# Performance work log

Measured on AMD Instinct MI355X. Metric: run time of the kernel, lower is better.

## Reference

```python
import jax, jax.numpy as jnp
import numpy as np
from jax import lax

B, S, H = 32, 512, 128
NEG_INF = -1e30  # matches util.masked_softmax's large negative fill


def setup_inputs() -> dict:
    key = jax.random.key(0)
    ks = jax.random.split(key, 10)
    sc = 0.05
    vp = jax.random.normal(ks[0], (B, S, 2 * H), dtype=jnp.float32)
    # valid lengths in [S//2, S]; packed loop runs max(lengths) steps
    p_s_lengths = jax.random.randint(ks[1], (B,), S // 2, S + 1, dtype=jnp.int32)
    W_vP  = jax.random.normal(ks[2], (H, 2 * H), dtype=jnp.float32) * sc      # linear_vP.weight
    W_vPt = jax.random.normal(ks[3], (H, 2 * H), dtype=jnp.float32) * sc      # linear_vPt.weight
    w_vT  = jax.random.normal(ks[4], (H,), dtype=jnp.float32) * sc            # linear_vT.weight (1,H) -> vector
    W_g   = jax.random.normal(ks[5], (4 * H, 4 * H), dtype=jnp.float32) * sc  # g.weight
    W_ih  = jax.random.normal(ks[6], (3 * H, 4 * H), dtype=jnp.float32) * sc  # GRUCell.weight_ih
    W_hh  = jax.random.normal(ks[7], (3 * H, H), dtype=jnp.float32) * sc      # GRUCell.weight_hh
    b_ih  = jax.random.normal(ks[8], (3 * H,), dtype=jnp.float32) * sc
    b_hh  = jax.random.normal(ks[9], (3 * H,), dtype=jnp.float32) * sc
    return dict(vp=vp, p_s_lengths=p_s_lengths, W_vP=W_vP, W_vPt=W_vPt,
                w_vT=w_vT, W_g=W_g, W_ih=W_ih, W_hh=W_hh, b_ih=b_ih, b_hh=b_hh)


def _self_attn_rnn(vp, p_s_lengths, W_vP, W_vPt, w_vT, W_g, W_ih, W_hh, b_ih, b_hh):
    Bb, Ss, H2 = vp.shape
    Hh = H2 // 2
    s_idx = jnp.arange(Ss)

    # reverse_enc: reverse each sequence only over its valid prefix
    rev_idx = jnp.where(s_idx[None, :] < p_s_lengths[:, None],
                        p_s_lengths[:, None] - 1 - s_idx[None, :], s_idx[None, :])
    rev_vp = jnp.take_along_axis(vp, rev_idx[:, :, None], axis=1)

    bidir_vp = jnp.concatenate([vp, rev_vp], axis=0)       # (2B,S,2H) inputs per step
    vp2 = jnp.concatenate([vp, vp], axis=0)                 # (2B,S,2H) attention memory (forward order!)
    len2 = jnp.concatenate([p_s_lengths, p_s_lengths], 0)   # (2B,)

    keyp = jnp.einsum('bsd,hd->bsh', vp2, W_vP)             # precompute linear_vP(vp)
    seq_mask = s_idx[None, :] < len2[:, None]               # (2B,S)

    def step(h, inputs):
        x_t, active = inputs                                # (2B,2H), (2B,)
        q = x_t @ W_vPt.T                                   # (2B,H)
        logits = jnp.tanh(keyp + q[:, None, :]) @ w_vT      # (2B,S)
        a = jax.nn.softmax(jnp.where(seq_mask, logits, NEG_INF), axis=1)
        ct = jnp.einsum('bs,bsd->bd', a, vp2)               # (2B,2H)
        vpc = jnp.concatenate([x_t, ct], axis=-1)           # (2B,4H)
        gt = jax.nn.sigmoid(vpc @ W_g.T)
        xin = gt * vpc
        gi = xin @ W_ih.T + b_ih
        gh = h @ W_hh.T + b_hh
        ir, iz, inn = jnp.split(gi, 3, axis=-1)
        hr, hz, hn = jnp.split(gh, 3, axis=-1)
        r = jax.nn.sigmoid(ir + hr)
        z = jax.nn.sigmoid(iz + hz)
        n = jnp.tanh(inn + r * hn)
        h_new = (1.0 - z) * n + z * h
        # packed semantics: inactive (padded) slots keep zeros and never update again
        h_new = jnp.where(active[:, None], h_new, 0.0)
        return h_new, h_new

    xs = (jnp.swapaxes(bidir_vp, 0, 1), seq_mask.T)          # (S,2B,2H), (S,2B)
    h0 = jnp.zeros((2 * Bb, Hh), dtype=vp.dtype)
    _, hs = lax.scan(jax.checkpoint(step), h0, xs)           # hs: (S,2B,H)
    hp = jnp.swapaxes(hs, 0, 1)                              # (2B,S,H)
    # original concatenates fwd half and rev half on feature dim (rev half stays in reversed time order)
    return jnp.concatenate([hp[:Bb], hp[Bb:]], axis=-1)      # (B,S,2H)


def reference(vp, p_s_lengths, W_vP, W_vPt, w_vT, W_g, W_ih, W_hh, b_ih, b_hh):
    # dropout is identity at inference (training=False)
    return _self_attn_rnn(vp, p_s_lengths, W_vP, W_vPt, w_vT, W_g, W_ih, W_hh, b_ih, b_hh)
```

## Files before the change

### kernel.cpp

```cpp
#include <hip/hip_runtime.h>
#include <hip/hip_fp16.h>

#define BB 32
#define SS 512
#define HH 128
#define D2 256
#define D3 384
#define D4 512

#define OFF_TK  0
#define OFF_TQ  (OFF_TK + BB*SS*HH)
#define OFF_CT  (OFF_TQ + BB*SS*HH)
#define OFF_GI  (OFF_CT + BB*SS*D2)
#define OFF_F16 (OFF_GI + BB*SS*D3)
#define F16_WG  0
#define F16_WIH (F16_WG + D4*D4)
#define F16_W2  (F16_WIH + D3*D4)

typedef _Float16 f16x8 __attribute__((ext_vector_type(8)));
typedef _Float16 f16x4 __attribute__((ext_vector_type(4)));
typedef float    f32x4 __attribute__((ext_vector_type(4)));
typedef _Float16 h2_t  __attribute__((ext_vector_type(2)));

__device__ __forceinline__ float fast_tanh(float x) {
  float ax = fabsf(x);
  float e  = __expf(-2.0f * ax);
  float t  = __fdividef(1.0f - e, 1.0f + e);
  return x < 0.0f ? -t : t;
}
__device__ __forceinline__ float sigm(float x) {
  return __fdividef(1.0f, 1.0f + __expf(-x));
}

__global__ __launch_bounds__(256) void k0_prep(
    const float* __restrict__ Wg, const float* __restrict__ Wih,
    const float* __restrict__ Wvp, const float* __restrict__ Wvpt,
    float* __restrict__ ws) {
  int i = blockIdx.x * 256 + threadIdx.x;
  _Float16* f16b = (_Float16*)(ws + OFF_F16);
  if (i < D4 * D4) {
    f16b[F16_WG + i] = (_Float16)Wg[i];
  } else if (i < D4 * D4 + D3 * D4) {
    int j = i - D4 * D4;
    f16b[F16_WIH + j] = (_Float16)Wih[j];
  } else {
    int j = i - D4 * D4 - D3 * D4;
    f16b[F16_W2 + j] = (_Float16)(j < HH * D2 ? Wvp[j] : Wvpt[j - HH * D2]);
  }
}

__global__ __launch_bounds__(256, 2) void k1_keyq(const float* __restrict__ vp,
                                                  float* __restrict__ ws) {
  __shared__ __align__(16) _Float16 vpH[64 * 256];
  int tid = threadIdx.x;
  int rows0 = blockIdx.x * 64;

  #pragma unroll
  for (int i = 0; i < 8; ++i) {
    int u = tid + i * 256;
    int r = u >> 5, c8 = u & 31;
    const float* src = vp + (size_t)(rows0 + r) * D2 + c8 * 8;
    float4 a = *(const float4*)src;
    float4 b = *(const float4*)(src + 4);
    f16x8 h;
    h[0]=(_Float16)a.x; h[1]=(_Float16)a.y; h[2]=(_Float16)a.z; h[3]=(_Float16)a.w;
    h[4]=(_Float16)b.x; h[5]=(_Float16)b.y; h[6]=(_Float16)b.z; h[7]=(_Float16)b.w;
    *(f16x8*)(&vpH[r * 256 + (c8 ^ (r & 7)) * 8]) = h;
  }
  __syncthreads();

  const _Float16* W2 = (const _Float16*)(ws + OFF_F16) + F16_W2;
  int w = tid >> 6, l = tid & 63;
  int lr = l & 15, lk = (l >> 4) * 8;

  f32x4 acc[4][4];
  #pragma unroll
  for (int m = 0; m < 4; ++m)
    #pragma unroll
    for (int n = 0; n < 4; ++n) acc[m][n] = (f32x4){0.f, 0.f, 0.f, 0.f};

  for (int kc = 0; kc < 8; ++kc) {
    int k = kc * 32 + lk;
    f16x8 bf[4];
    #pragma unroll
    for (int n = 0; n < 4; ++n) {
      int r = n * 16 + lr;
      bf[n] = *(const f16x8*)(&vpH[r * 256 + (((k >> 3) ^ (r & 7))) * 8]);
    }
    #pragma unroll
    for (int m = 0; m < 4; ++m) {
      int c = w * 64 + m * 16 + lr;
      f16x8 af = *(const f16x8*)(W2 + (size_t)c * 256 + k);
      #pragma unroll
      for (int n = 0; n < 4; ++n)
        acc[m][n] = __builtin_amdgcn_mfma_f32_16x16x32_f16(af, bf[n], acc[m][n], 0, 0, 0);
    }
  }

  int b = rows0 >> 9;
  int s0 = rows0 & 511;
  float* ekT = ws + OFF_TK + (size_t)b * HH * SS;
  float* eqp = ws + OFF_TQ + (size_t)b * SS * HH;
  #pragma unroll
  for (int m = 0; m < 4; ++m) {
    int c0 = w * 64 + m * 16 + (l >> 4) * 4;
    #pragma unroll
    for (int n = 0; n < 4; ++n) {
      int s = s0 + n * 16 + lr;
      float v[4];
      #pragma unroll
      for (int j = 0; j < 4; ++j) {
        float z = fminf(fmaxf(2.0f * acc[m][n][j], -60.0f), 60.0f);
        v[j] = __expf(z);
      }
      if (c0 < HH) {
        #pragma unroll
        for (int j = 0; j < 4; ++j)
          ekT[(size_t)(c0 + j) * SS + s] = v[j];
      } else {
        float4 o; o.x = v[0]; o.y = v[1]; o.z = v[2]; o.w = v[3];
        *(float4*)(eqp + (size_t)s * HH + (c0 - HH)) = o;
      }
    }
  }
}

__global__ __launch_bounds__(256) void k2_attn(const float* __restrict__ vp,
                                               const int* __restrict__ lens,
                                               const float* __restrict__ wvt,
                                               float* __restrict__ ws) {
  int bid = blockIdx.x;
  int b  = (bid & 7) * 4 + ((bid >> 3) & 3);
  int t0 = (bid >> 5) * 16;
  int len = lens[b];
  if (t0 >= len) return;
  int nt = min(16, len - t0);

  __shared__ float L[16][SS];
  __shared__ float Eqs[16][HH];
  __shared__ float inv_sum[16];

  int tid = threadIdx.x;
  const float* EkT = ws + OFF_TK + (size_t)b * HH * SS;
  const float* Eq  = ws + OFF_TQ + (size_t)b * SS * HH;

  for (int idx = tid; idx < 16 * HH; idx += 256) {
    int i = idx >> 7, h = idx & 127;
    Eqs[i][h] = Eq[(size_t)(t0 + i) * HH + h];
  }
  __syncthreads();

  for (int sc = 0; sc < 2; ++sc) {
    int s = tid + sc * 256;
    if (s < len) {
      float acc[16] = {};
      for (int h4 = 0; h4 < 32; ++h4) {
        float k0 = EkT[(size_t)(h4 * 4 + 0) * SS + s];
        float k1 = EkT[(size_t)(h4 * 4 + 1) * SS + s];
        float k2v = EkT[(size_t)(h4 * 4 + 2) * SS + s];
        float k3 = EkT[(size_t)(h4 * 4 + 3) * SS + s];
        const float4 w4 = *(const float4*)(wvt + h4 * 4);
        #pragma unroll
        for (int t = 0; t < 16; ++t) {
          const float4 q4 = *(const float4*)(&Eqs[t][h4 * 4]);
          float r0 = __builtin_amdgcn_rcpf(fmaf(k0, q4.x, 1.0f));
          float r1 = __builtin_amdgcn_rcpf(fmaf(k1, q4.y, 1.0f));
          float r2 = __builtin_amdgcn_rcpf(fmaf(k2v, q4.z, 1.0f));
          float r3 = __builtin_amdgcn_rcpf(fmaf(k3, q4.w, 1.0f));
          float a = acc[t];
          a = fmaf(w4.x, r0, a);
          a = fmaf(w4.y, r1, a);
          a = fmaf(w4.z, r2, a);
          a = fmaf(w4.w, r3, a);
          acc[t] = a;
        }
      }
      #pragma unroll
      for (int t = 0; t < 16; ++t) L[t][s] = -2.0f * acc[t];
    }
  }
  __syncthreads();

  {
    int w = tid >> 6, lane = tid & 63;
    for (int ii = 0; ii < 4; ++ii) {
      int i = w + ii * 4;
      if (i < nt) {
        float m = -1e30f;
        for (int s = lane; s < len; s += 64) m = fmaxf(m, L[i][s]);
        #pragma unroll
        for (int off = 32; off > 0; off >>= 1) m = fmaxf(m, __shfl_xor(m, off));
        float sm = 0.0f;
        for (int s = lane; s < len; s += 64) {
          float e = __expf(L[i][s] - m);
          L[i][s] = e;
          sm += e;
        }
        #pragma unroll
        for (int off = 32; off > 0; off >>= 1) sm += __shfl_xor(sm, off);
        if (lane == 0) inv_sum[i] = __fdividef(1.0f, sm);
      }
    }
  }
  __syncthreads();

  int d4 = (tid & 63) * 4;
  int tg = tid >> 6;
  float4 acc4[4] = {};
  const float* vpb = vp + (size_t)b * SS * D2;
  int s = 0;
  for (; s + 4 <= len; s += 4) {
    #pragma unroll
    for (int u = 0; u < 4; ++u) {
      float4 v4 = *(const float4*)(vpb + (size_t)(s + u) * D2 + d4);
      #pragma unroll
      for (int j = 0; j < 4; ++j) {
        float p = L[tg * 4 + j][s + u];
        acc4[j].x = fmaf(p, v4.x, acc4[j].x);
        acc4[j].y = fmaf(p, v4.y, acc4[j].y);
        acc4[j].z = fmaf(p, v4.z, acc4[j].z);
        acc4[j].w = fmaf(p, v4.w, acc4[j].w);
      }
    }
  }
  for (; s < len; ++s) {
    float4 v4 = *(const float4*)(vpb + (size_t)s * D2 + d4);
    #pragma unroll
    for (int j = 0; j < 4; ++j) {
      float p = L[tg * 4 + j][s];
      acc4[j].x = fmaf(p, v4.x, acc4[j].x);
      acc4[j].y = fmaf(p, v4.y, acc4[j].y);
      acc4[j].z = fmaf(p, v4.z, acc4[j].z);
      acc4[j].w = fmaf(p, v4.w, acc4[j].w);
    }
  }
  float* ctg = ws + OFF_CT + ((size_t)b * SS + t0) * D2;
  #pragma unroll
  for (int j = 0; j < 4; ++j) {
    int t = tg * 4 + j;
    if (t < nt) {
      float is = inv_sum[t];
      float4 o;
      o.x = acc4[j].x * is; o.y = acc4[j].y * is;
      o.z = acc4[j].z * is; o.w = acc4[j].w * is;
      *(float4*)(ctg + (size_t)t * D2 + d4) = o;
    }
  }
}

__global__ __launch_bounds__(256, 2) void k3_gates(const float* __restrict__ vp,
                                                   const int* __restrict__ lens,
                                                   const float* __restrict__ bih,
                                                   float* __restrict__ ws) {
  int b = blockIdx.y;
  int len = lens[b];
  int t0 = blockIdx.x * 32;
  if (t0 >= len) return;

  __shared__ __align__(16) _Float16 vpcH[32 * 512];
  int tid = threadIdx.x;
  const float* ct = ws + OFF_CT;

  #pragma unroll
  for (int i = 0; i < 8; ++i) {
    int u = tid + i * 256;
    int r = u >> 6, c8 = u & 63;
    int c = c8 * 8;
    const float* src = (c < D2) ? (vp + ((size_t)b * SS + t0 + r) * D2 + c)
                                : (ct + ((size_t)b * SS + t0 + r) * D2 + (c - D2));
    float4 a = *(const float4*)src;
    float4 bb = *(const float4*)(src + 4);
    f16x8 h;
    h[0]=(_Float16)a.x;  h[1]=(_Float16)a.y;  h[2]=(_Float16)a.z;  h[3]=(_Float16)a.w;
    h[4]=(_Float16)bb.x; h[5]=(_Float16)bb.y; h[6]=(_Float16)bb.z; h[7]=(_Float16)bb.w;
    *(f16x8*)(&vpcH[r * 512 + (c8 ^ (r & 7)) * 8]) = h;
  }
  __syncthreads();

  const _Float16* WgH  = (const _Float16*)(ws + OFF_F16) + F16_WG;
  const _Float16* WihH = (const _Float16*)(ws + OFF_F16) + F16_WIH;
  int w = tid >> 6, l = tid & 63;
  int lr = l & 15, lk = (l >> 4) * 8;

  f32x4 acc[8][2];
  #pragma unroll
  for (int m = 0; m < 8; ++m) { acc[m][0] = (f32x4){0.f,0.f,0.f,0.f}; acc[m][1] = (f32x4){0.f,0.f,0.f,0.f}; }

  for (int kc = 0; kc < 16; ++kc) {
    int k = kc * 32 + lk;
    f16x8 bf[2];
    #pragma unroll
    for (int n = 0; n < 2; ++n) {
      int r = n * 16 + lr;
      bf[n] = *(const f16x8*)(&vpcH[r * 512 + (((k >> 3) ^ (r & 7))) * 8]);
    }
    #pragma unroll
    for (int m = 0; m < 8; ++m) {
      int c = w * 128 + m * 16 + lr;
      f16x8 af = *(const f16x8*)(WgH + (size_t)c * 512 + k);
      acc[m][0] = __builtin_amdgcn_mfma_f32_16x16x32_f16(af, bf[0], acc[m][0], 0, 0, 0);
      acc[m][1] = __builtin_amdgcn_mfma_f32_16x16x32_f16(af, bf[1], acc[m][1], 0, 0, 0);
    }
  }

  f16x4 xq[8][2];
  #pragma unroll
  for (int m = 0; m < 8; ++m) {
    int c0 = w * 128 + m * 16 + (l >> 4) * 4;
    #pragma unroll
    for (int n = 0; n < 2; ++n) {
      int r = n * 16 + lr;
      int ea = r * 512 + (((c0 >> 3) ^ (r & 7))) * 8 + (c0 & 7);
      f16x4 vq = *(const f16x4*)(&vpcH[ea]);
      f16x4 xo;
      #pragma unroll
      for (int j = 0; j < 4; ++j)
        xo[j] = (_Float16)(sigm(acc[m][n][j]) * (float)vq[j]);
      xq[m][n] = xo;
    }
  }
  __syncthreads();
  #pragma unroll
  for (int m = 0; m < 8; ++m) {
    int c0 = w * 128 + m * 16 + (l >> 4) * 4;
    #pragma unroll
    for (int n = 0; n < 2; ++n) {
      int r = n * 16 + lr;
      int ea = r * 512 + (((c0 >> 3) ^ (r & 7))) * 8 + (c0 & 7);
      *(f16x4*)(&vpcH[ea]) = xq[m][n];
    }
  }
  __syncthreads();

  f32x4 gacc[6][2];
  #pragma unroll
  for (int m = 0; m < 6; ++m) { gacc[m][0] = (f32x4){0.f,0.f,0.f,0.f}; gacc[m][1] = (f32x4){0.f,0.f,0.f,0.f}; }

  for (int kc = 0; kc < 16; ++kc) {
    int k = kc * 32 + lk;
    f16x8 bf[2];
    #pragma unroll
    for (int n = 0; n < 2; ++n) {
      int r = n * 16 + lr;
      bf[n] = *(const f16x8*)(&vpcH[r * 512 + (((k >> 3) ^ (r & 7))) * 8]);
    }
    #pragma unroll
    for (int m = 0; m < 6; ++m) {
      int c = w * 96 + m * 16 + lr;
      f16x8 af = *(const f16x8*)(WihH + (size_t)c * 512 + k);
      gacc[m][0] = __builtin_amdgcn_mfma_f32_16x16x32_f16(af, bf[0], gacc[m][0], 0, 0, 0);
      gacc[m][1] = __builtin_amdgcn_mfma_f32_16x16x32_f16(af, bf[1], gacc[m][1], 0, 0, 0);
    }
  }

  float* gig = ws + OFF_GI;
  #pragma unroll
  for (int m = 0; m < 6; ++m) {
    int c0 = w * 96 + m * 16 + (l >> 4) * 4;
    float4 bq = *(const float4*)(bih + c0);
    #pragma unroll
    for (int n = 0; n < 2; ++n) {
      int r = n * 16 + lr;
      float4 o;
      o.x = gacc[m][n][0] + bq.x;
      o.y = gacc[m][n][1] + bq.y;
      o.z = gacc[m][n][2] + bq.z;
      o.w = gacc[m][n][3] + bq.w;
      *(float4*)(gig + ((size_t)b * SS + t0 + r) * D3 + c0) = o;
    }
  }
}

__global__ __launch_bounds__(256, 1) void k4_scan(const float* __restrict__ whh,
                                                  const float* __restrict__ bhh,
                                                  const int* __restrict__ lens,
                                                  const float* __restrict__ ws,
                                                  float* __restrict__ out) {
  int bid = blockIdx.x;
  int xcd = bid & 7, dir = (bid >> 3) & 1, q = bid >> 4;
  int b = xcd * 4 + q;
  int len = lens[b];
  int tid = threadIdx.x;
  int wv = tid >> 6, l = tid & 63;
  int j = wv * 32 + (l & 31);
  int p = l >> 5;
  const float* gi = ws + OFF_GI + (size_t)b * SS * D3;

  h2_t w0[32], w1[32], w2[32];
  {
    const float* r0 = whh + (size_t)j * HH + p * 64;
    const float* r1 = whh + (size_t)(j + 128) * HH + p * 64;
    const float* r2 = whh + (size_t)(j + 256) * HH + p * 64;
    #pragma unroll
    for (int k = 0; k < 32; ++k) {
      w0[k] = h2_t{(_Float16)r0[2 * k], (_Float16)r0[2 * k + 1]};
      w1[k] = h2_t{(_Float16)r1[2 * k], (_Float16)r1[2 * k + 1]};
      w2[k] = h2_t{(_Float16)r2[2 * k], (_Float16)r2[2 * k + 1]};
    }
  }
  float bh0 = bhh[j], bh1 = bhh[j + 128], bh2 = bhh[j + 256];

  __shared__ __align__(16) _Float16 hbuf[2][128];
  if (tid < 128) hbuf[0][tid] = (_Float16)0.0f;
  float h_own = 0.0f;

  float* outb = out + (size_t)b * SS * D2 + dir * HH;

#define K4_BAR() do {                                                          \
    asm volatile("s_waitcnt lgkmcnt(0)" ::: "memory");                         \
    __builtin_amdgcn_s_barrier();                                              \
    __builtin_amdgcn_sched_barrier(0);                                         \
  } while (0)

#define K4_PF(gx0, gx1, gx2, tnext) do {                                       \
    if (p == 0) {                                                              \
      int tp = (tnext) < len ? (tnext) : (len - 1);                            \
      int tgp = dir ? (len - 1 - tp) : tp;                                     \
      const float* gp = gi + (size_t)tgp * D3;                                 \
      gx0 = gp[j]; gx1 = gp[j + 128]; gx2 = gp[j + 256];                       \
    }                                                                          \
  } while (0)

#define K4_STEP(gx0, gx1, gx2, tstep, PB) do {                                 \
    const f16x8* hb8 = (const f16x8*)&hbuf[PB][p * 64];                        \
    float a00 = 0.f, a01 = 0.f, a02 = 0.f, a03 = 0.f;                          \
    float a10 = 0.f, a11 = 0.f, a12 = 0.f, a13 = 0.f;                          \
    float a20 = 0.f, a21 = 0.f, a22 = 0.f, a23 = 0.f;                          \
    _Pragma("unroll")                                                          \
    for (int k8 = 0; k8 < 8; ++k8) {                                           \
      f16x8 hv = hb8[k8];                                                      \
      h2_t q0 = __builtin_shufflevector(hv, hv, 0, 1);                         \
      h2_t q1 = __builtin_shufflevector(hv, hv, 2, 3);                         \
      h2_t q2 = __builtin_shufflevector(hv, hv, 4, 5);                         \
      h2_t q3 = __builtin_shufflevector(hv, hv, 6, 7);                         \
      a00 = __builtin_amdgcn_fdot2(q0, w0[4 * k8 + 0], a00, false);            \
      a01 = __builtin_amdgcn_fdot2(q1, w0[4 * k8 + 1], a01, false);            \
      a02 = __builtin_amdgcn_fdot2(q2, w0[4 * k8 + 2], a02, false);            \
      a03 = __builtin_amdgcn_fdot2(q3, w0[4 * k8 + 3], a03, false);            \
      a10 = __builtin_amdgcn_fdot2(q0, w1[4 * k8 + 0], a10, false);            \
      a11 = __builtin_amdgcn_fdot2(q1, w1[4 * k8 + 1], a11, false);            \
      a12 = __builtin_amdgcn_fdot2(q2, w1[4 * k8 + 2], a12, false);            \
      a13 = __builtin_amdgcn_fdot2(q3, w1[4 * k8 + 3], a13, false);            \
      a20 = __builtin_amdgcn_fdot2(q0, w2[4 * k8 + 0], a20, false);            \
      a21 = __builtin_amdgcn_fdot2(q1, w2[4 * k8 + 1], a21, false);            \
      a22 = __builtin_amdgcn_fdot2(q2, w2[4 * k8 + 2], a22, false);            \
      a23 = __builtin_amdgcn_fdot2(q3, w2[4 * k8 + 3], a23, false);            \
    }                                                                          \
    float s0 = ((a00 + a01) + (a02 + a03));                                    \
    float s1 = ((a10 + a11) + (a12 + a13));                                    \
    float s2 = ((a20 + a21) + (a22 + a23));                                    \
    s0 += __shfl_xor(s0, 32);                                                  \
    s1 += __shfl_xor(s1, 32);                                                  \
    s2 += __shfl_xor(s2, 32);                                                  \
    if (p == 0) {                                                              \
      float r = sigm((gx0) + s0 + bh0);                                        \
      float z = sigm((gx1) + s1 + bh1);                                        \
      float n = fast_tanh(fmaf(r, s2 + bh2, (gx2)));                           \
      float hn = (1.0f - z) * n + z * h_own;                                   \
      h_own = hn;                                                              \
      outb[(size_t)(tstep) * D2 + j] = hn;                                     \
      hbuf[(PB) ^ 1][j] = (_Float16)hn;                                        \
    }                                                                          \
    K4_PF(gx0, gx1, gx2, (tstep) + 4);                                         \
    K4_BAR();                                                                  \
  } while (0)

  float gA0 = 0.f, gA1 = 0.f, gA2 = 0.f;
  float gB0 = 0.f, gB1 = 0.f, gB2 = 0.f;
  float gC0 = 0.f, gC1 = 0.f, gC2 = 0.f;
  float gD0 = 0.f, gD1 = 0.f, gD2 = 0.f;
  K4_PF(gA0, gA1, gA2, 0);
  K4_PF(gB0, gB1, gB2, 1);
  K4_PF(gC0, gC1, gC2, 2);
  K4_PF(gD0, gD1, gD2, 3);
  K4_BAR();

  int t = 0;
  while (t + 3 < len) {
    K4_STEP(gA0, gA1, gA2, t,     0);
    K4_STEP(gB0, gB1, gB2, t + 1, 1);
    K4_STEP(gC0, gC1, gC2, t + 2, 0);
    K4_STEP(gD0, gD1, gD2, t + 3, 1);
    t += 4;
  }
  if (t < len)     K4_STEP(gA0, gA1, gA2, t,     0);
  if (t + 1 < len) K4_STEP(gB0, gB1, gB2, t + 1, 1);
  if (t + 2 < len) K4_STEP(gC0, gC1, gC2, t + 2, 0);

#undef K4_STEP
#undef K4_PF
#undef K4_BAR
}

extern "C" void kernel_launch(void* const* d_in, const int* in_sizes, int n_in,
                              void* d_out, int out_size, void* d_ws, size_t ws_size,
                              hipStream_t stream) {
  const float* vp   = (const float*)d_in[0];
  const int*   lens = (const int*)d_in[1];
  const float* Wvp  = (const float*)d_in[2];
  const float* Wvpt = (const float*)d_in[3];
  const float* wvt  = (const float*)d_in[4];
  const float* Wg   = (const float*)d_in[5];
  const float* Wih  = (const float*)d_in[6];
  const float* Whh  = (const float*)d_in[7];
  const float* bih  = (const float*)d_in[8];
  const float* bhh  = (const float*)d_in[9];
  float* out = (float*)d_out;
  float* ws  = (float*)d_ws;

  hipMemsetAsync(d_out, 0, (size_t)out_size * sizeof(float), stream);

  k0_prep<<<2048, 256, 0, stream>>>(Wg, Wih, Wvp, Wvpt, ws);
  k1_keyq<<<BB * SS / 64, 256, 0, stream>>>(vp, ws);
  k2_attn<<<1024, 256, 0, stream>>>(vp, lens, wvt, ws);
  k3_gates<<<dim3(SS / 32, BB), 256, 0, stream>>>(vp, lens, bih, ws);
  k4_scan<<<64, 256, 0, stream>>>(Whh, bhh, lens, ws, out);
}
```

Measured before the change: 530.8 us.

## Process forward and reverse GRU directions in one scan block per batch

The recurrent scan kernel now runs both directions for a batch in a single workgroup, so it launches 32 blocks instead of 64. Each step does two independent dot-product sets over separate shared h buffers and shares one barrier between them. This halves the number of barriers per step pair and gives each step two independent chains to interleave for latency hiding. The cost is a longer per-step critical path and half as many CUs in use, so the scan's wall time may grow if the chains do not overlap well.

```diff
diff --git a/kernel.cpp b/kernel.cpp
--- a/kernel.cpp
+++ b/kernel.cpp
@@ -377,8 +377,7 @@
                                                   const float* __restrict__ ws,
                                                   float* __restrict__ out) {
   int bid = blockIdx.x;
-  int xcd = bid & 7, dir = (bid >> 3) & 1, q = bid >> 4;
-  int b = xcd * 4 + q;
+  int b = (bid & 7) * 4 + (bid >> 3);
   int len = lens[b];
   int tid = threadIdx.x;
   int wv = tid >> 6, l = tid & 63;
@@ -400,11 +399,12 @@
   }
   float bh0 = bhh[j], bh1 = bhh[j + 128], bh2 = bhh[j + 256];
 
-  __shared__ __align__(16) _Float16 hbuf[2][128];
-  if (tid < 128) hbuf[0][tid] = (_Float16)0.0f;
-  float h_own = 0.0f;
-
-  float* outb = out + (size_t)b * SS * D2 + dir * HH;
+  __shared__ __align__(16) _Float16 hbuf[2][2][128];
+  if (tid < 256) hbuf[tid >> 7][0][tid & 127] = (_Float16)0.0f;
+  float hF_own = 0.0f, hR_own = 0.0f;
+
+  float* outF = out + (size_t)b * SS * D2;
+  float* outR = outF + HH;
 
 #define K4_BAR() do {                                                          \
     asm volatile("s_waitcnt lgkmcnt(0)" ::: "memory");                         \
@@ -412,23 +412,24 @@
     __builtin_amdgcn_sched_barrier(0);                                         \
   } while (0)
 
-#define K4_PF(gx0, gx1, gx2, tnext) do {                                       \
+#define K4_PF2(fx0, fx1, fx2, rx0, rx1, rx2, tnext) do {                       \
     if (p == 0) {                                                              \
       int tp = (tnext) < len ? (tnext) : (len - 1);                            \
-      int tgp = dir ? (len - 1 - tp) : tp;                                     \
-      const float* gp = gi + (size_t)tgp * D3;                                 \
-      gx0 = gp[j]; gx1 = gp[j + 128]; gx2 = gp[j + 256];                       \
+      const float* gf = gi + (size_t)tp * D3;                                  \
+      const float* gr = gi + (size_t)(len - 1 - tp) * D3;                      \
+      fx0 = gf[j]; fx1 = gf[j + 128]; fx2 = gf[j + 256];                       \
+      rx0 = gr[j]; rx1 = gr[j + 128]; rx2 = gr[j + 256];                       \
     }                                                                          \
   } while (0)
 
-#define K4_STEP(gx0, gx1, gx2, tstep, PB) do {                                 \
-    const f16x8* hb8 = (const f16x8*)&hbuf[PB][p * 64];                        \
+#define K4_DOTS(HB, S0, S1, S2) do {                                           \
+    const f16x8* hb8_ = (const f16x8*)(HB);                                    \
     float a00 = 0.f, a01 = 0.f, a02 = 0.f, a03 = 0.f;                          \
     float a10 = 0.f, a11 = 0.f, a12 = 0.f, a13 = 0.f;                          \
     float a20 = 0.f, a21 = 0.f, a22 = 0.f, a23 = 0.f;                          \
     _Pragma("unroll")                                                          \
     for (int k8 = 0; k8 < 8; ++k8) {                                           \
-      f16x8 hv = hb8[k8];                                                      \
+      f16x8 hv = hb8_[k8];                                                     \
       h2_t q0 = __builtin_shufflevector(hv, hv, 0, 1);                         \
       h2_t q1 = __builtin_shufflevector(hv, hv, 2, 3);                         \
       h2_t q2 = __builtin_shufflevector(hv, hv, 4, 5);                         \
@@ -446,49 +447,62 @@
       a22 = __builtin_amdgcn_fdot2(q2, w2[4 * k8 + 2], a22, false);            \
       a23 = __builtin_amdgcn_fdot2(q3, w2[4 * k8 + 3], a23, false);            \
     }                                                                          \
-    float s0 = ((a00 + a01) + (a02 + a03));                                    \
-    float s1 = ((a10 + a11) + (a12 + a13));                                    \
-    float s2 = ((a20 + a21) + (a22 + a23));                                    \
-    s0 += __shfl_xor(s0, 32);                                                  \
-    s1 += __shfl_xor(s1, 32);                                                  \
-    s2 += __shfl_xor(s2, 32);                                                  \
+    S0 = ((a00 + a01) + (a02 + a03));                                          \
+    S1 = ((a10 + a11) + (a12 + a13));                                          \
+    S2 = ((a20 + a21) + (a22 + a23));                                          \
+  } while (0)
+
+#define K4_TAIL(S0, S1, S2, GX0, GX1, GX2, HOWN, OUTB, DIRI, tstep, PB) do {   \
+    S0 += __shfl_xor(S0, 32);                                                  \
+    S1 += __shfl_xor(S1, 32);                                                  \
+    S2 += __shfl_xor(S2, 32);                                                  \
     if (p == 0) {                                                              \
-      float r = sigm((gx0) + s0 + bh0);                                        \
-      float z = sigm((gx1) + s1 + bh1);                                        \
-      float n = fast_tanh(fmaf(r, s2 + bh2, (gx2)));                           \
-      float hn = (1.0f - z) * n + z * h_own;                                   \
-      h_own = hn;                                                              \
-      outb[(size_t)(tstep) * D2 + j] = hn;                                     \
-      hbuf[(PB) ^ 1][j] = (_Float16)hn;                                        \
+      float r = sigm((GX0) + S0 + bh0);                                        \
+      float z = sigm((GX1) + S1 + bh1);                                        \
+      float n = fast_tanh(fmaf(r, S2 + bh2, (GX2)));                           \
+      float hn = (1.0f - z) * n + z * (HOWN);                                  \
+      HOWN = hn;                                                               \
+      (OUTB)[(size_t)(tstep) * D2 + j] = hn;                                   \
+      hbuf[DIRI][(PB) ^ 1][j] = (_Float16)hn;                                  \
     }                                                                          \
-    K4_PF(gx0, gx1, gx2, (tstep) + 4);                                         \
+  } while (0)
+
+#define K4_STEP2(fx0, fx1, fx2, rx0, rx1, rx2, tstep, PB) do {                 \
+    float sF0, sF1, sF2, sR0, sR1, sR2;                                        \
+    K4_DOTS(&hbuf[0][PB][p * 64], sF0, sF1, sF2);                              \
+    K4_DOTS(&hbuf[1][PB][p * 64], sR0, sR1, sR2);                              \
+    K4_TAIL(sF0, sF1, sF2, fx0, fx1, fx2, hF_own, outF, 0, tstep, PB);         \
+    K4_TAIL(sR0, sR1, sR2, rx0, rx1, rx2, hR_own, outR, 1, tstep, PB);         \
+    K4_PF2(fx0, fx1, fx2, rx0, rx1, rx2, (tstep) + 4);                         \
     K4_BAR();                                                                  \
   } while (0)
 
-  float gA0 = 0.f, gA1 = 0.f, gA2 = 0.f;
-  float gB0 = 0.f, gB1 = 0.f, gB2 = 0.f;
-  float gC0 = 0.f, gC1 = 0.f, gC2 = 0.f;
-  float gD0 = 0.f, gD1 = 0.f, gD2 = 0.f;
-  K4_PF(gA0, gA1, gA2, 0);
-  K4_PF(gB0, gB1, gB2, 1);
-  K4_PF(gC0, gC1, gC2, 2);
-  K4_PF(gD0, gD1, gD2, 3);
+  float fA0 = 0.f, fA1 = 0.f, fA2 = 0.f, rA0 = 0.f, rA1 = 0.f, rA2 = 0.f;
+  float fB0 = 0.f, fB1 = 0.f, fB2 = 0.f, rB0 = 0.f, rB1 = 0.f, rB2 = 0.f;
+  float fC0 = 0.f, fC1 = 0.f, fC2 = 0.f, rC0 = 0.f, rC1 = 0.f, rC2 = 0.f;
+  float fD0 = 0.f, fD1 = 0.f, fD2 = 0.f, rD0 = 0.f, rD1 = 0.f, rD2 = 0.f;
+  K4_PF2(fA0, fA1, fA2, rA0, rA1, rA2, 0);
+  K4_PF2(fB0, fB1, fB2, rB0, rB1, rB2, 1);
+  K4_PF2(fC0, fC1, fC2, rC0, rC1, rC2, 2);
+  K4_PF2(fD0, fD1, fD2, rD0, rD1, rD2, 3);
   K4_BAR();
 
   int t = 0;
   while (t + 3 < len) {
-    K4_STEP(gA0, gA1, gA2, t,     0);
-    K4_STEP(gB0, gB1, gB2, t + 1, 1);
-    K4_STEP(gC0, gC1, gC2, t + 2, 0);
-    K4_STEP(gD0, gD1, gD2, t + 3, 1);
+    K4_STEP2(fA0, fA1, fA2, rA0, rA1, rA2, t,     0);
+    K4_STEP2(fB0, fB1, fB2, rB0, rB1, rB2, t + 1, 1);
+    K4_STEP2(fC0, fC1, fC2, rC0, rC1, rC2, t + 2, 0);
+    K4_STEP2(fD0, fD1, fD2, rD0, rD1, rD2, t + 3, 1);
     t += 4;
   }
-  if (t < len)     K4_STEP(gA0, gA1, gA2, t,     0);
-  if (t + 1 < len) K4_STEP(gB0, gB1, gB2, t + 1, 1);
-  if (t + 2 < len) K4_STEP(gC0, gC1, gC2, t + 2, 0);
-
-#undef K4_STEP
-#undef K4_PF
+  if (t < len)     K4_STEP2(fA0, fA1, fA2, rA0, rA1, rA2, t,     0);
+  if (t + 1 < len) K4_STEP2(fB0, fB1, fB2, rB0, rB1, rB2, t + 1, 1);
+  if (t + 2 < len) K4_STEP2(fC0, fC1, fC2, rC0, rC1, rC2, t + 2, 0);
+
+#undef K4_STEP2
+#undef K4_TAIL
+#undef K4_DOTS
+#undef K4_PF2
 #undef K4_BAR
 }
 
@@ -514,5 +528,5 @@
   k1_keyq<<<BB * SS / 64, 256, 0, stream>>>(vp, ws);
   k2_attn<<<1024, 256, 0, stream>>>(vp, lens, wvt, ws);
   k3_gates<<<dim3(SS / 32, BB), 256, 0, stream>>>(vp, lens, bih, ws);
-  k4_scan<<<64, 256, 0, stream>>>(Whh, bhh, lens, ws, out);
-}
+  k4_scan<<<32, 256, 0, stream>>>(Whh, bhh, lens, ws, out);
+}
```

New measurement: 787.3 us. +48.3%, slower.
